# Optimization experiments

Measured on AMD Instinct MI355X. Metric: run time of the kernel, lower is better.

The kernel has to match this reference:

```python
import jax, jax.numpy as jnp
import numpy as np

EPS = 1e-6

def setup_inputs() -> dict:
    key = jax.random.key(0)
    ks = jax.random.split(key, 4)
    T, B, D, N = 512, 16, 1024, 512
    # xavier-uniform-ish scale for projections
    lim = float(np.sqrt(6.0 / (N + D)))
    x = jax.random.normal(ks[0], (T, B, D), dtype=jnp.float32)
    W_k = jax.random.uniform(ks[1], (N, D), minval=-lim, maxval=lim, dtype=jnp.float32)
    W_v = jax.random.uniform(ks[2], (N, D), minval=-lim, maxval=lim, dtype=jnp.float32)
    W_q = jax.random.uniform(ks[3], (N, D), minval=-lim, maxval=lim, dtype=jnp.float32)
    return {"x": x, "W_k": W_k, "W_v": W_v, "W_q": W_q}

def reference(x, W_k, W_v, W_q):
    # x: (T, B, D); delta-rule fast-weight cell, proj=no_z, nonlin=tanh,
    # gate=output, update=delta.
    T, B, D = x.shape
    n = W_k.shape[0]
    k = jnp.einsum('tbd,nd->tbn', x, W_k)
    v = jnp.einsum('tbd,nd->tbn', x, W_v)
    q = jnp.einsum('tbd,nd->tbn', x, W_q)
    k_norm = k / (jnp.linalg.norm(k, axis=-1, keepdims=True) + EPS)

    def step(S, kvq):
        k_t, v_t, q_t = kvq  # each (B, n)
        retrieved = jnp.einsum('bij,bj->bi', S, k_t)
        delta = v_t - retrieved
        S_new = jnp.tanh(S + delta[:, :, None] * k_t[:, None, :])
        Sq = jnp.einsum('bij,bj->bi', S_new, q_t)
        out = Sq * jax.nn.silu(Sq)
        return S_new, out

    S0 = jnp.zeros((B, n, n), dtype=x.dtype)
    S_final, outputs = jax.lax.scan(step, S0, (k_norm, v, q))
    return outputs, S_final
```

## Files before the change

kernel.cpp:

```cpp
#include <hip/hip_runtime.h>
#include <hip/hip_bf16.h>

#define T_DIM 512
#define B_DIM 16
#define D_DIM 1024
#define N_DIM 512

#define C_FOLD  2.885390082f
#define INV_C   0.3465735903f

typedef short s16x8 __attribute__((ext_vector_type(8)));
typedef float f32x4 __attribute__((ext_vector_type(4)));
typedef float f32x2 __attribute__((ext_vector_type(2)));

__device__ __forceinline__ unsigned short f2bf(float f) {
    unsigned u = __float_as_uint(f);
    unsigned r = (u + 0x7fffu + ((u >> 16) & 1u)) >> 16;
    return (unsigned short)r;
}

__device__ __forceinline__ float half32_sum(float x) {
    x += __int_as_float(__builtin_amdgcn_update_dpp(0, __float_as_int(x), 0xB1,  0xf, 0xf, true));
    x += __int_as_float(__builtin_amdgcn_update_dpp(0, __float_as_int(x), 0x4E,  0xf, 0xf, true));
    x += __int_as_float(__builtin_amdgcn_update_dpp(0, __float_as_int(x), 0x124, 0xf, 0xf, true));
    x += __int_as_float(__builtin_amdgcn_update_dpp(0, __float_as_int(x), 0x128, 0xf, 0xf, true));
    x += __int_as_float(__builtin_amdgcn_ds_swizzle(__float_as_int(x), 0x401F));
    return x;
}

__global__ __launch_bounds__(256) void proj_gemm(
    const float* __restrict__ x,
    const float* __restrict__ Wk,
    const float* __restrict__ Wv,
    const float* __restrict__ Wq,
    float* __restrict__ kbuf, float* __restrict__ vbuf, float* __restrict__ qbuf)
{
    const float* W = (blockIdx.z == 0) ? Wk : (blockIdx.z == 1) ? Wv : Wq;
    float* out = (blockIdx.z == 0) ? kbuf : (blockIdx.z == 1) ? vbuf : qbuf;

    __shared__ __align__(16) unsigned short As[64 * 40];
    __shared__ __align__(16) unsigned short Bs[64 * 40];

    const int tid  = threadIdx.x;
    const int m0   = blockIdx.x * 64;
    const int n0   = blockIdx.y * 64;
    const int wave = tid >> 6;
    const int lane = tid & 63;
    const int l15  = lane & 15;
    const int quad = lane >> 4;

    const int srow = tid >> 2;
    const int scol = (tid & 3) * 8;

    f32x4 acc[4];
#pragma unroll
    for (int i = 0; i < 4; ++i) acc[i] = (f32x4)0.0f;

    for (int k0 = 0; k0 < D_DIM; k0 += 32) {
        __syncthreads();
        {
            const float* srcA = &x[(size_t)(m0 + srow) * D_DIM + k0 + scol];
            float4 a0 = *(const float4*)srcA;
            float4 a1 = *(const float4*)(srcA + 4);
            uint4 pa;
            pa.x = (unsigned)f2bf(a0.x) | ((unsigned)f2bf(a0.y) << 16);
            pa.y = (unsigned)f2bf(a0.z) | ((unsigned)f2bf(a0.w) << 16);
            pa.z = (unsigned)f2bf(a1.x) | ((unsigned)f2bf(a1.y) << 16);
            pa.w = (unsigned)f2bf(a1.z) | ((unsigned)f2bf(a1.w) << 16);
            *(uint4*)&As[srow * 40 + scol] = pa;

            const float* srcB = &W[(size_t)(n0 + srow) * D_DIM + k0 + scol];
            float4 b0 = *(const float4*)srcB;
            float4 b1 = *(const float4*)(srcB + 4);
            uint4 pb;
            pb.x = (unsigned)f2bf(b0.x) | ((unsigned)f2bf(b0.y) << 16);
            pb.y = (unsigned)f2bf(b0.z) | ((unsigned)f2bf(b0.w) << 16);
            pb.z = (unsigned)f2bf(b1.x) | ((unsigned)f2bf(b1.y) << 16);
            pb.w = (unsigned)f2bf(b1.z) | ((unsigned)f2bf(b1.w) << 16);
            *(uint4*)&Bs[srow * 40 + scol] = pb;
        }
        __syncthreads();
        s16x8 af = *(const s16x8*)&As[(wave * 16 + l15) * 40 + quad * 8];
#pragma unroll
        for (int nt = 0; nt < 4; ++nt) {
            s16x8 bf = *(const s16x8*)&Bs[(nt * 16 + l15) * 40 + quad * 8];
            acc[nt] = __builtin_amdgcn_mfma_f32_16x16x32_bf16(af, bf, acc[nt], 0, 0, 0);
        }
    }
#pragma unroll
    for (int nt = 0; nt < 4; ++nt) {
#pragma unroll
        for (int rg = 0; rg < 4; ++rg) {
            int row = m0 + wave * 16 + quad * 4 + rg;
            int col = n0 + nt * 16 + l15;
            out[(size_t)row * N_DIM + col] = acc[nt][rg];
        }
    }
}

__global__ __launch_bounds__(256) void knorm(float* __restrict__ kbuf)
{
    const int wave = threadIdx.x >> 6;
    const int lane = threadIdx.x & 63;
    const int row  = blockIdx.x * 4 + wave;
    float* p = &kbuf[(size_t)row * N_DIM + lane * 8];
    float4 a = *(const float4*)p;
    float4 b = *(const float4*)(p + 4);
    float s = a.x*a.x + a.y*a.y + a.z*a.z + a.w*a.w
            + b.x*b.x + b.y*b.y + b.z*b.z + b.w*b.w;
#pragma unroll
    for (int m = 1; m < 64; m <<= 1) s += __shfl_xor(s, m, 64);
    float inv = 1.0f / (sqrtf(s) + 1e-6f);
    a.x *= inv; a.y *= inv; a.z *= inv; a.w *= inv;
    b.x *= inv; b.y *= inv; b.z *= inv; b.w *= inv;
    *(float4*)p = a;
    *(float4*)(p + 4) = b;
}

__global__ __launch_bounds__(256) void scan_kernel(
    const float* __restrict__ kbuf, const float* __restrict__ vbuf,
    const float* __restrict__ qbuf, float* __restrict__ out)
{
    __shared__ __align__(16) float ks[2][576];
    __shared__ __align__(16) float qs[2][576];
    __shared__ float vs[2][8];

    const int tid  = threadIdx.x;
    const int lane = tid & 63;
    const int tj   = lane & 31;
    const int b    = blockIdx.y;
    const int i0   = blockIdx.x * 8;
    const int r0   = tid >> 5;

    const int wA = 36 * (tid >> 4) + ((2 * tid) & 31);
    const int rA = 36 * (tj >> 1) + 16 * (tj & 1);

    f32x2 SA[8];
#pragma unroll
    for (int u = 0; u < 8; ++u) SA[u] = (f32x2)0.0f;

    float2 pk, pq; float pv = 0.0f;
    {
        const size_t o0 = (size_t)b * N_DIM;
        pk = *(const float2*)&kbuf[o0 + 2 * tid];
        pq = *(const float2*)&qbuf[o0 + 2 * tid];
        if (tid < 8) pv = vbuf[o0 + i0 + tid];
        *(float2*)&ks[0][wA] = pk;
        *(float2*)&qs[0][wA] = pq;
        if (tid < 8) vs[0][tid] = pv;
        const size_t o1 = (size_t)(B_DIM + b) * N_DIM;
        pk = *(const float2*)&kbuf[o1 + 2 * tid];
        pq = *(const float2*)&qbuf[o1 + 2 * tid];
        if (tid < 8) pv = vbuf[o1 + i0 + tid];
    }
    __syncthreads();

    const f32x2 Cv   = {C_FOLD, C_FOLD};
    const f32x2 M2Cv = {-2.0f * C_FOLD, -2.0f * C_FOLD};

    for (int t = 0; t < T_DIM; ++t) {
        const int cb = t & 1, nb = cb ^ 1;
        const size_t ofs = ((size_t)t * B_DIM + b) * N_DIM;

        if (t + 1 < T_DIM) {
            *(float2*)&ks[nb][wA] = pk;
            *(float2*)&qs[nb][wA] = pq;
            if (tid < 8) vs[nb][tid] = pv;
        }
        if (t + 2 < T_DIM) {
            const size_t o2 = ((size_t)(t + 2) * B_DIM + b) * N_DIM;
            pk = *(const float2*)&kbuf[o2 + 2 * tid];
            pq = *(const float2*)&qbuf[o2 + 2 * tid];
            if (tid < 8) pv = vbuf[o2 + i0 + tid];
        }

        f32x2 k2[8], q2[8];
#pragma unroll
        for (int u = 0; u < 4; ++u) {
            f32x4 kv = *(const f32x4*)&ks[cb][rA + 4 * u];
            f32x4 qv = *(const f32x4*)&qs[cb][rA + 4 * u];
            k2[2*u] = kv.xy; k2[2*u+1] = kv.zw;
            q2[2*u] = qv.xy; q2[2*u+1] = qv.zw;
        }
        const float v0 = vs[cb][r0];

        f32x2 pa = (f32x2)0.0f, pb = (f32x2)0.0f;
#pragma unroll
        for (int u = 0; u < 8; u += 2) {
            pa += SA[u]     * k2[u];
            pb += SA[u + 1] * k2[u + 1];
        }
        const float racc = half32_sum(pa.x + pa.y + pb.x + pb.y);

        const float dp = __builtin_fmaf(C_FOLD, v0, -racc);
        const f32x2 d0 = {dp, dp};

        f32x2 sa = (f32x2)0.0f, sb = (f32x2)0.0f;
#pragma unroll
        for (int u = 0; u < 8; u += 2) {
            f32x2 a0 = SA[u]     + d0 * k2[u];
            f32x2 a1 = SA[u + 1] + d0 * k2[u + 1];
            f32x2 e0 = { __builtin_amdgcn_exp2f(a0.x), __builtin_amdgcn_exp2f(a0.y) };
            f32x2 e1 = { __builtin_amdgcn_exp2f(a1.x), __builtin_amdgcn_exp2f(a1.y) };
            e0 = e0 + 1.0f; e1 = e1 + 1.0f;
            f32x2 rc0 = { __builtin_amdgcn_rcpf(e0.x), __builtin_amdgcn_rcpf(e0.y) };
            f32x2 rc1 = { __builtin_amdgcn_rcpf(e1.x), __builtin_amdgcn_rcpf(e1.y) };
            f32x2 n0 = Cv + rc0 * M2Cv;
            f32x2 n1 = Cv + rc1 * M2Cv;
            SA[u] = n0; SA[u + 1] = n1;
            sa += n0 * q2[u];
            sb += n1 * q2[u + 1];
        }
        const float sq = half32_sum(sa.x + sa.y + sb.x + sb.y);

        if (tj == 0) {
            float s0 = sq * INV_C;
            float g0 = __builtin_amdgcn_rcpf(1.0f + __builtin_amdgcn_exp2f(-s0 * 1.44269504f));
            out[ofs + i0 + r0] = s0 * s0 * g0;
        }
        __syncthreads();
    }

    const size_t base = (size_t)T_DIM * B_DIM * N_DIM;
    const size_t so0 = base + ((size_t)b * N_DIM + i0 + r0) * N_DIM + 16 * tj;
#pragma unroll
    for (int u = 0; u < 4; ++u) {
        float4 w0;
        w0.x = SA[2*u].x   * INV_C; w0.y = SA[2*u].y   * INV_C;
        w0.z = SA[2*u+1].x * INV_C; w0.w = SA[2*u+1].y * INV_C;
        *(float4*)&out[so0 + 4 * u] = w0;
    }
}

extern "C" void kernel_launch(void* const* d_in, const int* in_sizes, int n_in,
                              void* d_out, int out_size, void* d_ws, size_t ws_size,
                              hipStream_t stream) {
    const float* x  = (const float*)d_in[0];
    const float* Wk = (const float*)d_in[1];
    const float* Wv = (const float*)d_in[2];
    const float* Wq = (const float*)d_in[3];
    float* outp = (float*)d_out;

    const size_t MN = (size_t)T_DIM * B_DIM * N_DIM;
    float* kbuf = (float*)d_ws;
    float* vbuf = kbuf + MN;
    float* qbuf = vbuf + MN;

    proj_gemm<<<dim3(128, 8, 3), 256, 0, stream>>>(x, Wk, Wv, Wq, kbuf, vbuf, qbuf);
    knorm<<<2048, 256, 0, stream>>>(kbuf);
    scan_kernel<<<dim3(64, 16), 256, 0, stream>>>(kbuf, vbuf, qbuf, outp);
}
```

Measured before the change: 807.1 us.

## Give each scan thread 32 state columns and batch reciprocals across eight values

The scan kernel now assigns 16 rows per block and 32 state columns per thread, so row reductions span 16 lanes and need only DPP steps, without the ds_swizzle. The grid is halved to 512 blocks. The tanh update uses Montgomery batch inversion, replacing eight rcp instructions with one rcp plus multiplies, to cut transcendental throughput cost. Pointer increments replace per-step offset math. The costs are more registers per thread, fewer blocks on the GPU, and possible precision loss or overflow in the product of the eight (1+exp) terms.

```diff
diff --git a/kernel.cpp b/kernel.cpp
--- a/kernel.cpp
+++ b/kernel.cpp
@@ -19,12 +19,11 @@
     return (unsigned short)r;
 }
 
-__device__ __forceinline__ float half32_sum(float x) {
+__device__ __forceinline__ float reduce16(float x) {
     x += __int_as_float(__builtin_amdgcn_update_dpp(0, __float_as_int(x), 0xB1,  0xf, 0xf, true));
     x += __int_as_float(__builtin_amdgcn_update_dpp(0, __float_as_int(x), 0x4E,  0xf, 0xf, true));
     x += __int_as_float(__builtin_amdgcn_update_dpp(0, __float_as_int(x), 0x124, 0xf, 0xf, true));
     x += __int_as_float(__builtin_amdgcn_update_dpp(0, __float_as_int(x), 0x128, 0xf, 0xf, true));
-    x += __int_as_float(__builtin_amdgcn_ds_swizzle(__float_as_int(x), 0x401F));
     return x;
 }
 
@@ -123,112 +122,138 @@
 {
     __shared__ __align__(16) float ks[2][576];
     __shared__ __align__(16) float qs[2][576];
-    __shared__ float vs[2][8];
-
-    const int tid  = threadIdx.x;
-    const int lane = tid & 63;
-    const int tj   = lane & 31;
-    const int b    = blockIdx.y;
-    const int i0   = blockIdx.x * 8;
-    const int r0   = tid >> 5;
-
-    const int wA = 36 * (tid >> 4) + ((2 * tid) & 31);
-    const int rA = 36 * (tj >> 1) + 16 * (tj & 1);
-
-    f32x2 SA[8];
-#pragma unroll
-    for (int u = 0; u < 8; ++u) SA[u] = (f32x2)0.0f;
+    __shared__ float vs[2][16];
+
+    const int tid = threadIdx.x;
+    const int l4  = tid & 15;
+    const int g   = tid >> 4;
+    const int b   = blockIdx.y;
+    const int i0  = blockIdx.x * 16;
+
+    const int wA  = 36 * (tid >> 4) + ((2 * tid) & 31);
+    const int rA2 = 36 * l4;
+
+    f32x2 S2[16];
+#pragma unroll
+    for (int u = 0; u < 16; ++u) S2[u] = (f32x2)0.0f;
+
+    const int DT = B_DIM * N_DIM;
+    const float* kp = kbuf + (size_t)b * N_DIM + 2 * tid;
+    const float* qp = qbuf + (size_t)b * N_DIM + 2 * tid;
+    const float* vp = vbuf + (size_t)b * N_DIM + i0 + tid;
 
     float2 pk, pq; float pv = 0.0f;
     {
-        const size_t o0 = (size_t)b * N_DIM;
-        pk = *(const float2*)&kbuf[o0 + 2 * tid];
-        pq = *(const float2*)&qbuf[o0 + 2 * tid];
-        if (tid < 8) pv = vbuf[o0 + i0 + tid];
+        pk = *(const float2*)kp; kp += DT;
+        pq = *(const float2*)qp; qp += DT;
+        if (tid < 16) pv = *vp;
+        vp += DT;
         *(float2*)&ks[0][wA] = pk;
         *(float2*)&qs[0][wA] = pq;
-        if (tid < 8) vs[0][tid] = pv;
-        const size_t o1 = (size_t)(B_DIM + b) * N_DIM;
-        pk = *(const float2*)&kbuf[o1 + 2 * tid];
-        pq = *(const float2*)&qbuf[o1 + 2 * tid];
-        if (tid < 8) pv = vbuf[o1 + i0 + tid];
+        if (tid < 16) vs[0][tid] = pv;
+        pk = *(const float2*)kp; kp += DT;
+        pq = *(const float2*)qp; qp += DT;
+        if (tid < 16) pv = *vp;
+        vp += DT;
     }
     __syncthreads();
+
+    float* op = out + (size_t)b * N_DIM + i0 + g;
 
     const f32x2 Cv   = {C_FOLD, C_FOLD};
     const f32x2 M2Cv = {-2.0f * C_FOLD, -2.0f * C_FOLD};
 
     for (int t = 0; t < T_DIM; ++t) {
         const int cb = t & 1, nb = cb ^ 1;
-        const size_t ofs = ((size_t)t * B_DIM + b) * N_DIM;
 
         if (t + 1 < T_DIM) {
             *(float2*)&ks[nb][wA] = pk;
             *(float2*)&qs[nb][wA] = pq;
-            if (tid < 8) vs[nb][tid] = pv;
+            if (tid < 16) vs[nb][tid] = pv;
         }
         if (t + 2 < T_DIM) {
-            const size_t o2 = ((size_t)(t + 2) * B_DIM + b) * N_DIM;
-            pk = *(const float2*)&kbuf[o2 + 2 * tid];
-            pq = *(const float2*)&qbuf[o2 + 2 * tid];
-            if (tid < 8) pv = vbuf[o2 + i0 + tid];
-        }
-
-        f32x2 k2[8], q2[8];
-#pragma unroll
-        for (int u = 0; u < 4; ++u) {
-            f32x4 kv = *(const f32x4*)&ks[cb][rA + 4 * u];
-            f32x4 qv = *(const f32x4*)&qs[cb][rA + 4 * u];
+            pk = *(const float2*)kp;
+            pq = *(const float2*)qp;
+            if (tid < 16) pv = *vp;
+        }
+        kp += DT; qp += DT; vp += DT;
+
+        f32x2 k2[16], q2[16];
+#pragma unroll
+        for (int u = 0; u < 8; ++u) {
+            f32x4 kv = *(const f32x4*)&ks[cb][rA2 + 4 * u];
+            f32x4 qv = *(const f32x4*)&qs[cb][rA2 + 4 * u];
             k2[2*u] = kv.xy; k2[2*u+1] = kv.zw;
             q2[2*u] = qv.xy; q2[2*u+1] = qv.zw;
         }
-        const float v0 = vs[cb][r0];
-
-        f32x2 pa = (f32x2)0.0f, pb = (f32x2)0.0f;
-#pragma unroll
-        for (int u = 0; u < 8; u += 2) {
-            pa += SA[u]     * k2[u];
-            pb += SA[u + 1] * k2[u + 1];
-        }
-        const float racc = half32_sum(pa.x + pa.y + pb.x + pb.y);
+        const float v0 = vs[cb][g];
+
+        f32x2 p0 = (f32x2)0.0f, p1 = (f32x2)0.0f;
+        f32x2 p2 = (f32x2)0.0f, p3 = (f32x2)0.0f;
+#pragma unroll
+        for (int w = 0; w < 4; ++w) {
+            p0 += S2[4*w]     * k2[4*w];
+            p1 += S2[4*w + 1] * k2[4*w + 1];
+            p2 += S2[4*w + 2] * k2[4*w + 2];
+            p3 += S2[4*w + 3] * k2[4*w + 3];
+        }
+        p0 += p1; p2 += p3; p0 += p2;
+        const float racc = reduce16(p0.x + p0.y);
 
         const float dp = __builtin_fmaf(C_FOLD, v0, -racc);
         const f32x2 d0 = {dp, dp};
 
-        f32x2 sa = (f32x2)0.0f, sb = (f32x2)0.0f;
-#pragma unroll
-        for (int u = 0; u < 8; u += 2) {
-            f32x2 a0 = SA[u]     + d0 * k2[u];
-            f32x2 a1 = SA[u + 1] + d0 * k2[u + 1];
-            f32x2 e0 = { __builtin_amdgcn_exp2f(a0.x), __builtin_amdgcn_exp2f(a0.y) };
-            f32x2 e1 = { __builtin_amdgcn_exp2f(a1.x), __builtin_amdgcn_exp2f(a1.y) };
-            e0 = e0 + 1.0f; e1 = e1 + 1.0f;
-            f32x2 rc0 = { __builtin_amdgcn_rcpf(e0.x), __builtin_amdgcn_rcpf(e0.y) };
-            f32x2 rc1 = { __builtin_amdgcn_rcpf(e1.x), __builtin_amdgcn_rcpf(e1.y) };
-            f32x2 n0 = Cv + rc0 * M2Cv;
-            f32x2 n1 = Cv + rc1 * M2Cv;
-            SA[u] = n0; SA[u + 1] = n1;
-            sa += n0 * q2[u];
-            sb += n1 * q2[u + 1];
-        }
-        const float sq = half32_sum(sa.x + sa.y + sb.x + sb.y);
-
-        if (tj == 0) {
+        f32x2 sacc0 = (f32x2)0.0f, sacc1 = (f32x2)0.0f;
+#pragma unroll
+        for (int w = 0; w < 4; ++w) {
+            f32x2 a0 = S2[4*w]     + d0 * k2[4*w];
+            f32x2 a1 = S2[4*w + 1] + d0 * k2[4*w + 1];
+            f32x2 a2 = S2[4*w + 2] + d0 * k2[4*w + 2];
+            f32x2 a3 = S2[4*w + 3] + d0 * k2[4*w + 3];
+            f32x2 f0 = { __builtin_amdgcn_exp2f(a0.x), __builtin_amdgcn_exp2f(a0.y) };
+            f32x2 f1 = { __builtin_amdgcn_exp2f(a1.x), __builtin_amdgcn_exp2f(a1.y) };
+            f32x2 f2 = { __builtin_amdgcn_exp2f(a2.x), __builtin_amdgcn_exp2f(a2.y) };
+            f32x2 f3 = { __builtin_amdgcn_exp2f(a3.x), __builtin_amdgcn_exp2f(a3.y) };
+            f0 = f0 + 1.0f; f1 = f1 + 1.0f; f2 = f2 + 1.0f; f3 = f3 + 1.0f;
+            f32x2 m0 = f0 * f1;
+            f32x2 m1 = f2 * f3;
+            f32x2 qq = m0 * m1;
+            float rP = __builtin_amdgcn_rcpf(qq.x * qq.y);
+            f32x2 rq  = { qq.y * rP, qq.x * rP };
+            f32x2 rm0 = rq * m1;
+            f32x2 rm1 = rq * m0;
+            f32x2 r0 = rm0 * f1;
+            f32x2 r1 = rm0 * f0;
+            f32x2 r2 = rm1 * f3;
+            f32x2 r3 = rm1 * f2;
+            f32x2 n0 = Cv + r0 * M2Cv;
+            f32x2 n1 = Cv + r1 * M2Cv;
+            f32x2 n2 = Cv + r2 * M2Cv;
+            f32x2 n3 = Cv + r3 * M2Cv;
+            S2[4*w] = n0; S2[4*w + 1] = n1; S2[4*w + 2] = n2; S2[4*w + 3] = n3;
+            sacc0 += n0 * q2[4*w]     + n2 * q2[4*w + 2];
+            sacc1 += n1 * q2[4*w + 1] + n3 * q2[4*w + 3];
+        }
+        sacc0 += sacc1;
+        const float sq = reduce16(sacc0.x + sacc0.y);
+
+        if (l4 == 0) {
             float s0 = sq * INV_C;
             float g0 = __builtin_amdgcn_rcpf(1.0f + __builtin_amdgcn_exp2f(-s0 * 1.44269504f));
-            out[ofs + i0 + r0] = s0 * s0 * g0;
-        }
+            op[0] = s0 * s0 * g0;
+        }
+        op += DT;
         __syncthreads();
     }
 
     const size_t base = (size_t)T_DIM * B_DIM * N_DIM;
-    const size_t so0 = base + ((size_t)b * N_DIM + i0 + r0) * N_DIM + 16 * tj;
-#pragma unroll
-    for (int u = 0; u < 4; ++u) {
+    const size_t so = base + ((size_t)b * N_DIM + i0 + g) * N_DIM + 32 * l4;
+#pragma unroll
+    for (int u = 0; u < 8; ++u) {
         float4 w0;
-        w0.x = SA[2*u].x   * INV_C; w0.y = SA[2*u].y   * INV_C;
-        w0.z = SA[2*u+1].x * INV_C; w0.w = SA[2*u+1].y * INV_C;
-        *(float4*)&out[so0 + 4 * u] = w0;
+        w0.x = S2[2*u].x   * INV_C; w0.y = S2[2*u].y   * INV_C;
+        w0.z = S2[2*u+1].x * INV_C; w0.w = S2[2*u+1].y * INV_C;
+        *(float4*)&out[so + 4 * u] = w0;
     }
 }
 
@@ -248,5 +273,5 @@
 
     proj_gemm<<<dim3(128, 8, 3), 256, 0, stream>>>(x, Wk, Wv, Wq, kbuf, vbuf, qbuf);
     knorm<<<2048, 256, 0, stream>>>(kbuf);
-    scan_kernel<<<dim3(64, 16), 256, 0, stream>>>(kbuf, vbuf, qbuf, outp);
-}
+    scan_kernel<<<dim3(32, 16), 256, 0, stream>>>(kbuf, vbuf, qbuf, outp);
+}
```

New measurement: 704.9 us. 1.15x faster.
